# Performance work log

Measured on AMD Instinct MI355X. Metric: run time of the kernel, lower is better.

## Reference

```python
import jax, jax.numpy as jnp
import numpy as np

EPS = 1e-6
NUM_HEADS = 32
HEAD_DIM = 128


def _rms_norm(x, w):
    # RMSNorm over last dim (head_dim)
    var = jnp.mean(x * x, axis=-1, keepdims=True)
    return x * jax.lax.rsqrt(var + EPS) * w


def _rotate_half(x):
    x1, x2 = jnp.split(x, 2, axis=-1)
    return jnp.concatenate([-x2, x1], axis=-1)


def _apply_rope(x, cos, sin):
    # x: [b, t, h, d]; cos/sin: [t, d] -> broadcast over batch and heads
    c = cos[None, :, None, :]
    s = sin[None, :, None, :]
    return x * c + _rotate_half(x) * s


def setup_inputs() -> dict:
    key = jax.random.key(0)
    ks = jax.random.split(key, 7)
    b, q_len, ctx_len, hidden = 4, 64, 4096, 4096
    total = ctx_len + q_len
    return {
        "hidden_states": jax.random.normal(ks[0], (b, q_len, hidden), jnp.float32),
        "target_hidden": jax.random.normal(ks[1], (b, ctx_len, hidden), jnp.float32),
        "cos": jax.random.uniform(ks[2], (total, HEAD_DIM), jnp.float32, -1.0, 1.0),
        "sin": jax.random.uniform(ks[3], (total, HEAD_DIM), jnp.float32, -1.0, 1.0),
        "Wqkv": jax.random.normal(ks[4], (hidden, 3 * hidden), jnp.float32) * 0.02,
        "Wo": jax.random.normal(ks[5], (hidden, hidden), jnp.float32) * 0.02,
        "q_norm_w": jnp.ones((HEAD_DIM,), jnp.float32),
    }


def reference(hidden_states, target_hidden, cos, sin, Wqkv, Wo, q_norm_w):
    b, q_len, hidden = hidden_states.shape
    ctx_len = target_hidden.shape[1]
    H, D = NUM_HEADS, HEAD_DIM

    # fused QKV projection; only the query slice is consumed (per source)
    qkv = jnp.einsum("bqh,hz->bqz", hidden_states, Wqkv)
    q = qkv[..., : H * D].reshape(b, q_len, H, D)

    # q_norm is applied twice in the source forward
    q = _rms_norm(_rms_norm(q, q_norm_w), q_norm_w)

    # KV built by concatenating raw target_hidden context with draft hidden states
    kv = jnp.concatenate([target_hidden, hidden_states], axis=1)  # [b, ctx+q, hidden]
    k = kv.reshape(b, ctx_len + q_len, H, D)
    v = k  # v = k view per source (rope applied only to k)

    # rotary: draft queries occupy positions ctx_len .. ctx_len+q_len-1
    q = _apply_rope(q, cos[ctx_len:], sin[ctx_len:])
    k = _apply_rope(k, cos, sin)

    # attention (full attention of draft queries over context + draft keys)
    scale = 1.0 / jnp.sqrt(jnp.asarray(D, q.dtype))
    scores = jnp.einsum("bqhd,bkhd->bhqk", q, k) * scale
    probs = jax.nn.softmax(scores, axis=-1)
    out = jnp.einsum("bhqk,bkhd->bqhd", probs, v)

    out = out.reshape(b, q_len, H * D)
    return jnp.einsum("bqh,ho->bqo", out, Wo)
```

## Files before the change

kernel.cpp:

```cpp
#include <hip/hip_runtime.h>

typedef __attribute__((ext_vector_type(8))) short bf16x8;
typedef __attribute__((ext_vector_type(4))) float f32x4;
typedef __attribute__((ext_vector_type(4))) short s16x4;

#define DEV __device__ __forceinline__

DEV short f2bf(float f) {
  union { float f; unsigned u; } v; v.f = f;
  unsigned r = v.u + 0x7fffu + ((v.u >> 16) & 1u);
  return (short)(r >> 16);
}

DEV int pk2(float a, float b) {
#if defined(__has_builtin) && __has_builtin(__builtin_amdgcn_cvt_pk_bf16_f32)
  auto v = __builtin_amdgcn_cvt_pk_bf16_f32(a, b);
  int r; __builtin_memcpy(&r, &v, 4); return r;
#else
  return (int)(unsigned short)f2bf(a) | ((int)(unsigned short)f2bf(b) << 16);
#endif
}

DEV void stage16(const short* g, short* lbase, int lane) {
#if defined(__has_builtin) && __has_builtin(__builtin_amdgcn_global_load_lds)
  (void)lane;
  __builtin_amdgcn_global_load_lds((const __attribute__((address_space(1))) void*)g,
                                   (__attribute__((address_space(3))) void*)lbase, 16, 0, 0);
#else
  *(bf16x8*)(lbase + lane * 8) = *(const bf16x8*)g;
#endif
}

DEV void stage16f(const float* g, float* lbase, int lane) {
#if defined(__has_builtin) && __has_builtin(__builtin_amdgcn_global_load_lds)
  (void)lane;
  __builtin_amdgcn_global_load_lds((const __attribute__((address_space(1))) void*)g,
                                   (__attribute__((address_space(3))) void*)lbase, 16, 0, 0);
#else
  *(float4*)(lbase + lane * 4) = *(const float4*)g;
#endif
}

__global__ __launch_bounds__(256) void prep_w(
    const float* __restrict__ wqkv, const float* __restrict__ wo,
    short* __restrict__ out) {
  __shared__ short tile[64][66];
  int z = blockIdx.z;
  const float* in = z ? wo : wqkv;
  long ld = z ? 4096 : 12288;
  short* o = out + (long)z * 16777216L;
  long k0 = blockIdx.x * 64L, n0 = blockIdx.y * 64L;
  int t = threadIdx.x;
  {
    int kl = t >> 4, nl4 = (t & 15) * 4;
#pragma unroll
    for (int i = 0; i < 4; i++) {
      int k = kl + i * 16;
      float4 v = *(const float4*)(in + (k0 + k) * ld + n0 + nl4);
      int* dst = (int*)&tile[k][nl4];
      dst[0] = pk2(v.x, v.y);
      dst[1] = pk2(v.z, v.w);
    }
  }
  __syncthreads();
  {
    int nl = t >> 4, kl4 = (t & 15) * 4;
#pragma unroll
    for (int i = 0; i < 4; i++) {
      int n = nl + i * 16;
      s16x4 w;
      w.x = tile[kl4 + 0][n]; w.y = tile[kl4 + 1][n];
      w.z = tile[kl4 + 2][n]; w.w = tile[kl4 + 3][n];
      *(s16x4*)(o + (n0 + n) * 4096L + k0 + kl4) = w;
    }
  }
}

__global__ __launch_bounds__(256) void cast_f32_bf16(
    const float* __restrict__ in, short* __restrict__ out, int n8,
    float* __restrict__ zbuf) {
  int i = blockIdx.x * 256 + threadIdx.x;
  if (i >= n8) return;
  float4 a = *(const float4*)(in + (long)i * 8);
  float4 b = *(const float4*)(in + (long)i * 8 + 4);
  union { bf16x8 v; int w[4]; } r;
  r.w[0] = pk2(a.x, a.y); r.w[1] = pk2(a.z, a.w);
  r.w[2] = pk2(b.x, b.y); r.w[3] = pk2(b.z, b.w);
  *(bf16x8*)(out + (long)i * 8) = r.v;
  float4 z4 = make_float4(0.f, 0.f, 0.f, 0.f);
  *(float4*)(zbuf + (long)i * 8) = z4;
  *(float4*)(zbuf + (long)i * 8 + 4) = z4;
}

__global__ __launch_bounds__(512) void gemm_dma(
    const short* __restrict__ A, const short* __restrict__ Bt,
    float* __restrict__ Cp, int N, int K, int Kc) {
  __shared__ short As[32 * 512];
  __shared__ short Bs[8 * 512];
  int t = threadIdx.x;
  int lane = t & 63, wave = t >> 6;
  int quad = lane >> 4, m16 = lane & 15;
  long n0 = blockIdx.x * 64L;
  int z = blockIdx.y;
  f32x4 acc[2][4] = {};
  int kbeg = z * Kc, kend = kbeg + Kc;

  for (int k0 = kbeg; k0 < kend; k0 += 64) {
    __syncthreads();
#pragma unroll
    for (int i = 0; i < 2; i++)
#pragma unroll
      for (int s = 0; s < 2; s++) {
        int row = (2 * wave + i) * 16 + m16;
        const short* g = A + (long)row * K + k0 + (s * 4 + quad) * 8;
        stage16(g, &As[(4 * wave + 2 * i + s) * 512], lane);
      }
    {
      int nt = wave >> 1, s = wave & 1;
      long row = n0 + nt * 16 + m16;
      const short* g = Bt + row * (long)K + k0 + (s * 4 + quad) * 8;
      stage16(g, &Bs[wave * 512], lane);
    }
    __syncthreads();
#pragma unroll
    for (int s = 0; s < 2; s++) {
      bf16x8 a0 = *(bf16x8*)&As[(4 * wave + s) * 512 + lane * 8];
      bf16x8 a1 = *(bf16x8*)&As[(4 * wave + 2 + s) * 512 + lane * 8];
#pragma unroll
      for (int nt = 0; nt < 4; nt++) {
        bf16x8 b = *(bf16x8*)&Bs[(nt * 2 + s) * 512 + lane * 8];
        acc[0][nt] = __builtin_amdgcn_mfma_f32_16x16x32_bf16(a0, b, acc[0][nt], 0, 0, 0);
        acc[1][nt] = __builtin_amdgcn_mfma_f32_16x16x32_bf16(a1, b, acc[1][nt], 0, 0, 0);
      }
    }
  }
  float* C = Cp + (long)z * 256 * N;
#pragma unroll
  for (int i = 0; i < 2; i++)
#pragma unroll
    for (int nt = 0; nt < 4; nt++)
#pragma unroll
      for (int rg = 0; rg < 4; rg++) {
        long m = (2 * wave + i) * 16 + quad * 4 + rg;
        C[m * (long)N + n0 + nt * 16 + m16] = acc[i][nt][rg];
      }
}

__global__ __launch_bounds__(512) void gemm_dma_atomic(
    const short* __restrict__ A, const short* __restrict__ Bt,
    float* __restrict__ C, int N, int K, int Kc) {
  __shared__ short As[32 * 512];
  __shared__ short Bs[8 * 512];
  int t = threadIdx.x;
  int lane = t & 63, wave = t >> 6;
  int quad = lane >> 4, m16 = lane & 15;
  long n0 = blockIdx.x * 64L;
  int z = blockIdx.y;
  f32x4 acc[2][4] = {};
  int kbeg = z * Kc, kend = kbeg + Kc;

  for (int k0 = kbeg; k0 < kend; k0 += 64) {
    __syncthreads();
#pragma unroll
    for (int i = 0; i < 2; i++)
#pragma unroll
      for (int s = 0; s < 2; s++) {
        int row = (2 * wave + i) * 16 + m16;
        const short* g = A + (long)row * K + k0 + (s * 4 + quad) * 8;
        stage16(g, &As[(4 * wave + 2 * i + s) * 512], lane);
      }
    {
      int nt = wave >> 1, s = wave & 1;
      long row = n0 + nt * 16 + m16;
      const short* g = Bt + row * (long)K + k0 + (s * 4 + quad) * 8;
      stage16(g, &Bs[wave * 512], lane);
    }
    __syncthreads();
#pragma unroll
    for (int s = 0; s < 2; s++) {
      bf16x8 a0 = *(bf16x8*)&As[(4 * wave + s) * 512 + lane * 8];
      bf16x8 a1 = *(bf16x8*)&As[(4 * wave + 2 + s) * 512 + lane * 8];
#pragma unroll
      for (int nt = 0; nt < 4; nt++) {
        bf16x8 b = *(bf16x8*)&Bs[(nt * 2 + s) * 512 + lane * 8];
        acc[0][nt] = __builtin_amdgcn_mfma_f32_16x16x32_bf16(a0, b, acc[0][nt], 0, 0, 0);
        acc[1][nt] = __builtin_amdgcn_mfma_f32_16x16x32_bf16(a1, b, acc[1][nt], 0, 0, 0);
      }
    }
  }
#pragma unroll
  for (int i = 0; i < 2; i++)
#pragma unroll
    for (int nt = 0; nt < 4; nt++)
#pragma unroll
      for (int rg = 0; rg < 4; rg++) {
        long m = (2 * wave + i) * 16 + quad * 4 + rg;
        unsafeAtomicAdd(&C[m * (long)N + n0 + nt * 16 + m16], acc[i][nt][rg]);
      }
}

__global__ __launch_bounds__(256) void q_norm_rope(
    const float* __restrict__ qtmp, const float* __restrict__ qw,
    const float* __restrict__ cosp, const float* __restrict__ sinp,
    short* __restrict__ qr) {
  int wid = blockIdx.x * 4 + (threadIdx.x >> 6);
  int lane = threadIdx.x & 63;
  int rrow = wid >> 5, h = wid & 31;
  long base = (long)rrow * 4096 + h * 128;
  const long STR = 256L * 4096;
  float x1 = 0.f, x2 = 0.f;
#pragma unroll
  for (int z = 0; z < 8; z++) {
    x1 += qtmp[z * STR + base + lane];
    x2 += qtmp[z * STR + base + 64 + lane];
  }
  float w1 = qw[lane], w2 = qw[64 + lane];
  float ss = x1 * x1 + x2 * x2;
#pragma unroll
  for (int m = 1; m < 64; m <<= 1) ss += __shfl_xor(ss, m, 64);
  float rs = rsqrtf(ss * (1.0f / 128.0f) + 1e-6f);
  float y1 = x1 * rs * w1, y2 = x2 * rs * w2;
  float ss2 = y1 * y1 + y2 * y2;
#pragma unroll
  for (int m = 1; m < 64; m <<= 1) ss2 += __shfl_xor(ss2, m, 64);
  float rs2 = rsqrtf(ss2 * (1.0f / 128.0f) + 1e-6f);
  float z1 = y1 * rs2 * w1, z2 = y2 * rs2 * w2;
  long cpos = (long)(4096 + (rrow & 63)) * 128;
  float c1 = cosp[cpos + lane], c2 = cosp[cpos + 64 + lane];
  float s1 = sinp[cpos + lane], s2 = sinp[cpos + 64 + lane];
  const float scale = 0.08838834764831845f;
  float o1 = (z1 * c1 - z2 * s1) * scale;
  float o2 = (z2 * c2 + z1 * s2) * scale;
  qr[base + lane] = f2bf(o1);
  qr[base + 64 + lane] = f2bf(o2);
}

#define ATT_SPLIT 7
#define ATT_TILES 10

__global__ __launch_bounds__(256) void attn_kernel(
    const short* __restrict__ qr, const float* __restrict__ th,
    const float* __restrict__ hs, const float* __restrict__ cosp,
    const float* __restrict__ sinp, float* __restrict__ part,
    float* __restrict__ mstat, float* __restrict__ lstat) {
  __shared__ short Ks[64 * 136];
  __shared__ short Vt[128 * 80];
  __shared__ short Ps[64 * 72];
  __shared__ float Xraw[64 * 128];
  int bh = blockIdx.x, split = blockIdx.y;
  int b = bh >> 5, h = bh & 31;
  int t = threadIdx.x;
  int wave = t >> 6, lane = t & 63, quad = lane >> 4, m16 = lane & 15;

  int tile0 = split * ATT_TILES;
  int ntiles = (65 - tile0 < ATT_TILES) ? (65 - tile0) : ATT_TILES;

  bf16x8 aq[4];
  {
    const short* qrow = qr + (long)(b * 64 + wave * 16 + m16) * 4096 + h * 128;
#pragma unroll
    for (int s = 0; s < 4; s++) aq[s] = *(const bf16x8*)(qrow + s * 32 + quad * 8);
  }
  float mi[4] = {-INFINITY, -INFINITY, -INFINITY, -INFINITY};
  float li[4] = {0.f, 0.f, 0.f, 0.f};
  f32x4 oacc[8] = {};

  int srow = t >> 2;
  int sc = t & 3;
  int colw = srow ^ (sc * 16);

  {
    int tl = tile0;
#pragma unroll
    for (int j = 0; j < 8; j++) {
      int r = (wave * 8 + j) * 2 + (lane >> 5);
      int lgn = tl * 64 + r;
      int cs = lane & 31;
      int fo = (cs ^ (r & 7)) << 2;
      const float* src = (lgn < 4096)
          ? th + ((long)b * 4096 + lgn) * 4096 + h * 128 + fo
          : hs + ((long)b * 64 + (lgn - 4096)) * 4096 + h * 128 + fo;
      stage16f(src, &Xraw[(wave * 8 + j) * 256], lane);
    }
  }

  for (int tt = 0; tt < ntiles; tt++) {
    int lg = (tile0 + tt) * 64 + srow;
    __syncthreads();
    {
      const float* crow = cosp + (long)lg * 128;
      const float* srw = sinp + (long)lg * 128;
      const float* xrow = Xraw + srow * 128;
      int sx = srow & 7;
#pragma unroll
      for (int i = 0; i < 2; i++) {
        int c = sc + 4 * i;
        int d1 = c * 8, d2 = d1 + 64;
        int c0 = c * 2;
        alignas(16) float xa[8], xb[8], cA[8], sA[8], cB[8], sB[8];
        *(float4*)&xa[0] = *(const float4*)(xrow + ((c0 ^ sx) << 2));
        *(float4*)&xa[4] = *(const float4*)(xrow + (((c0 + 1) ^ sx) << 2));
        *(float4*)&xb[0] = *(const float4*)(xrow + (((c0 + 16) ^ sx) << 2));
        *(float4*)&xb[4] = *(const float4*)(xrow + (((c0 + 17) ^ sx) << 2));
        *(float4*)&cA[0] = *(const float4*)(crow + d1);
        *(float4*)&cA[4] = *(const float4*)(crow + d1 + 4);
        *(float4*)&cB[0] = *(const float4*)(crow + d2);
        *(float4*)&cB[4] = *(const float4*)(crow + d2 + 4);
        *(float4*)&sA[0] = *(const float4*)(srw + d1);
        *(float4*)&sA[4] = *(const float4*)(srw + d1 + 4);
        *(float4*)&sB[0] = *(const float4*)(srw + d2);
        *(float4*)&sB[4] = *(const float4*)(srw + d2 + 4);
        union { bf16x8 v; int w[4]; } K1, K2;
#pragma unroll
        for (int jj = 0; jj < 4; jj++) {
          int j0 = 2 * jj, j1 = 2 * jj + 1;
          K1.w[jj] = pk2(xa[j0] * cA[j0] - xb[j0] * sA[j0],
                         xa[j1] * cA[j1] - xb[j1] * sA[j1]);
          K2.w[jj] = pk2(xb[j0] * cB[j0] + xa[j0] * sB[j0],
                         xb[j1] * cB[j1] + xa[j1] * sB[j1]);
        }
        *(bf16x8*)&Ks[srow * 136 + d1] = K1.v;
        *(bf16x8*)&Ks[srow * 136 + d2] = K2.v;
#pragma unroll
        for (int jj = 0; jj < 4; jj++) {
          int p1 = pk2(xa[2 * jj], xa[2 * jj + 1]);
          int p2 = pk2(xb[2 * jj], xb[2 * jj + 1]);
          Vt[(d1 + 2 * jj) * 80 + colw] = (short)(p1 & 0xffff);
          Vt[(d1 + 2 * jj + 1) * 80 + colw] = (short)((unsigned)p1 >> 16);
          Vt[(d2 + 2 * jj) * 80 + colw] = (short)(p2 & 0xffff);
          Vt[(d2 + 2 * jj + 1) * 80 + colw] = (short)((unsigned)p2 >> 16);
        }
      }
    }
    __syncthreads();

    if (tt + 1 < ntiles) {
      int tl = tile0 + tt + 1;
#pragma unroll
      for (int j = 0; j < 8; j++) {
        int r = (wave * 8 + j) * 2 + (lane >> 5);
        int lgn = tl * 64 + r;
        int cs = lane & 31;
        int fo = (cs ^ (r & 7)) << 2;
        const float* src = (lgn < 4096)
            ? th + ((long)b * 4096 + lgn) * 4096 + h * 128 + fo
            : hs + ((long)b * 64 + (lgn - 4096)) * 4096 + h * 128 + fo;
        stage16f(src, &Xraw[(wave * 8 + j) * 256], lane);
      }
    }

    f32x4 sacc[4] = {};
#pragma unroll
    for (int s = 0; s < 4; s++)
#pragma unroll
      for (int nt = 0; nt < 4; nt++) {
        bf16x8 bk = *(const bf16x8*)&Ks[(nt * 16 + m16) * 136 + s * 32 + quad * 8];
        sacc[nt] = __builtin_amdgcn_mfma_f32_16x16x32_bf16(aq[s], bk, sacc[nt], 0, 0, 0);
      }

    float mnew[4], alpha[4];
#pragma unroll
    for (int rg = 0; rg < 4; rg++) {
      float mx = fmaxf(fmaxf(sacc[0][rg], sacc[1][rg]), fmaxf(sacc[2][rg], sacc[3][rg]));
#pragma unroll
      for (int msk = 1; msk < 16; msk <<= 1) mx = fmaxf(mx, __shfl_xor(mx, msk, 16));
      mnew[rg] = fmaxf(mi[rg], mx);
      alpha[rg] = __expf(mi[rg] - mnew[rg]);
      mi[rg] = mnew[rg];
    }
#pragma unroll
    for (int rg = 0; rg < 4; rg++) {
      float rs = 0.f;
#pragma unroll
      for (int nt = 0; nt < 4; nt++) {
        float p = __expf(sacc[nt][rg] - mnew[rg]);
        rs += p;
        Ps[(wave * 16 + quad * 4 + rg) * 72 + nt * 16 + m16] = f2bf(p);
      }
#pragma unroll
      for (int msk = 1; msk < 16; msk <<= 1) rs += __shfl_xor(rs, msk, 16);
      li[rg] = li[rg] * alpha[rg] + rs;
    }
#pragma unroll
    for (int nt = 0; nt < 8; nt++) {
      f32x4 o = oacc[nt];
      o[0] *= alpha[0]; o[1] *= alpha[1]; o[2] *= alpha[2]; o[3] *= alpha[3];
      oacc[nt] = o;
    }

    bf16x8 ap[2];
#pragma unroll
    for (int s = 0; s < 2; s++)
      ap[s] = *(const bf16x8*)&Ps[(wave * 16 + m16) * 72 + s * 32 + quad * 8];
#pragma unroll
    for (int s = 0; s < 2; s++)
#pragma unroll
      for (int nt = 0; nt < 8; nt++) {
        int d16 = nt * 16 + m16;
        int scd = (d16 >> 3) & 3;
        int cb = (s * 32 + quad * 8) ^ (scd * 16);
        bf16x8 bv = *(const bf16x8*)&Vt[d16 * 80 + cb];
        oacc[nt] = __builtin_amdgcn_mfma_f32_16x16x32_bf16(ap[s], bv, oacc[nt], 0, 0, 0);
      }
  }

  long pbase = (long)(bh * ATT_SPLIT + split) * 64;
#pragma unroll
  for (int nt = 0; nt < 8; nt++)
#pragma unroll
    for (int rg = 0; rg < 4; rg++)
      part[(pbase + wave * 16 + quad * 4 + rg) * 128 + nt * 16 + m16] = oacc[nt][rg];
  if (m16 == 0)
#pragma unroll
    for (int rg = 0; rg < 4; rg++) {
      mstat[pbase + wave * 16 + quad * 4 + rg] = mi[rg];
      lstat[pbase + wave * 16 + quad * 4 + rg] = li[rg];
    }
}

__global__ __launch_bounds__(128) void attn_merge(
    const float* __restrict__ part, const float* __restrict__ mstat,
    const float* __restrict__ lstat, short* __restrict__ attn) {
  int idx = blockIdx.x;
  int bh = idx >> 6, q = idx & 63;
  int d = threadIdx.x;
  float mstar = -INFINITY;
#pragma unroll
  for (int s = 0; s < ATT_SPLIT; s++)
    mstar = fmaxf(mstar, mstat[((long)bh * ATT_SPLIT + s) * 64 + q]);
  float denom = 0.f, o = 0.f;
#pragma unroll
  for (int s = 0; s < ATT_SPLIT; s++) {
    long sq = ((long)bh * ATT_SPLIT + s) * 64 + q;
    float w = __expf(mstat[sq] - mstar);
    denom += w * lstat[sq];
    o += w * part[sq * 128 + d];
  }
  int b = bh >> 5, h = bh & 31;
  attn[(long)(b * 64 + q) * 4096 + h * 128 + d] = f2bf(o / denom);
}

extern "C" void kernel_launch(void* const* d_in, const int* in_sizes, int n_in,
                              void* d_out, int out_size, void* d_ws, size_t ws_size,
                              hipStream_t stream) {
  const float* hs = (const float*)d_in[0];
  const float* th = (const float*)d_in[1];
  const float* cosp = (const float*)d_in[2];
  const float* sinp = (const float*)d_in[3];
  const float* wqkv = (const float*)d_in[4];
  const float* wo = (const float*)d_in[5];
  const float* qw = (const float*)d_in[6];
  float* out = (float*)d_out;

  char* ws = (char*)d_ws;
  short* WT   = (short*)ws;
  short* hsb  = (short*)(ws + (64L << 20));
  float* qtmp = (float*)(ws + (66L << 20));
  short* qrb  = (short*)(ws + (98L << 20));
  short* attnb= (short*)(ws + (100L << 20));
  float* part = (float*)(ws + (102L << 20));
  float* mstat= (float*)(ws + (131L << 20));
  float* lstat= (float*)(ws + (132L << 20));

  prep_w<<<dim3(64, 64, 2), 256, 0, stream>>>(wqkv, wo, WT);
  cast_f32_bf16<<<512, 256, 0, stream>>>(hs, hsb, 131072, out);
  gemm_dma<<<dim3(64, 8), 512, 0, stream>>>(hsb, WT, qtmp, 4096, 4096, 512);
  q_norm_rope<<<2048, 256, 0, stream>>>(qtmp, qw, cosp, sinp, qrb);
  attn_kernel<<<dim3(128, ATT_SPLIT), 256, 0, stream>>>(qrb, th, hs, cosp, sinp,
                                                        part, mstat, lstat);
  attn_merge<<<128 * 64, 128, 0, stream>>>(part, mstat, lstat, attnb);
  gemm_dma_atomic<<<dim3(64, 8), 512, 0, stream>>>(attnb, WT + 16777216L, out,
                                                   4096, 4096, 512);
}
```

Before: 631.5 us.

## Double-buffer split-K GEMM with atomics, remap blocks across XCDs, rebalance attention splits

The split-K GEMM now double-buffers its LDS tiles so the next K-chunk loads while MFMAs run on the current one. Both GEMMs accumulate through atomics into a zeroed buffer, which removes the 8-way partial buffer and the summation in q_norm_rope. Block IDs are remapped so consecutive blocks land on the same XCD, and attention goes from 7 splits of 10 tiles to 4 splits of 17. This trades extra LDS and atomic traffic for fewer partial writes and better overlap, and the remap assumes attn_merge handles the new split count.

```diff
diff --git a/kernel.cpp b/kernel.cpp
--- a/kernel.cpp
+++ b/kernel.cpp
@@ -78,7 +78,7 @@
 
 __global__ __launch_bounds__(256) void cast_f32_bf16(
     const float* __restrict__ in, short* __restrict__ out, int n8,
-    float* __restrict__ zbuf) {
+    float* __restrict__ z1, float* __restrict__ z2) {
   int i = blockIdx.x * 256 + threadIdx.x;
   if (i >= n8) return;
   float4 a = *(const float4*)(in + (long)i * 8);
@@ -88,106 +88,64 @@
   r.w[2] = pk2(b.x, b.y); r.w[3] = pk2(b.z, b.w);
   *(bf16x8*)(out + (long)i * 8) = r.v;
   float4 z4 = make_float4(0.f, 0.f, 0.f, 0.f);
-  *(float4*)(zbuf + (long)i * 8) = z4;
-  *(float4*)(zbuf + (long)i * 8 + 4) = z4;
-}
-
-__global__ __launch_bounds__(512) void gemm_dma(
+  *(float4*)(z1 + (long)i * 8) = z4;
+  *(float4*)(z1 + (long)i * 8 + 4) = z4;
+  *(float4*)(z2 + (long)i * 8) = z4;
+  *(float4*)(z2 + (long)i * 8 + 4) = z4;
+}
+
+__global__ __launch_bounds__(512) void gemm_dma_at(
     const short* __restrict__ A, const short* __restrict__ Bt,
-    float* __restrict__ Cp, int N, int K, int Kc) {
-  __shared__ short As[32 * 512];
-  __shared__ short Bs[8 * 512];
+    float* __restrict__ C, int N, int K, int Kc) {
+  __shared__ short As[2][32 * 512];
+  __shared__ short Bs[2][8 * 512];
   int t = threadIdx.x;
   int lane = t & 63, wave = t >> 6;
   int quad = lane >> 4, m16 = lane & 15;
-  long n0 = blockIdx.x * 64L;
-  int z = blockIdx.y;
+  int sid = (blockIdx.x & 7) * 64 + (blockIdx.x >> 3);
+  int z = sid >> 6;
+  long n0 = (sid & 63) * 64L;
   f32x4 acc[2][4] = {};
-  int kbeg = z * Kc, kend = kbeg + Kc;
-
-  for (int k0 = kbeg; k0 < kend; k0 += 64) {
+  int kbeg = z * Kc;
+  int niter = Kc / 64;
+
+#define GSTAGE(B, K0)                                                        \
+  {                                                                          \
+    _Pragma("unroll")                                                        \
+    for (int i = 0; i < 2; i++)                                              \
+      _Pragma("unroll")                                                      \
+      for (int s = 0; s < 2; s++) {                                          \
+        int row = (2 * wave + i) * 16 + m16;                                 \
+        const short* g = A + (long)row * K + (K0) + (s * 4 + quad) * 8;      \
+        stage16(g, &As[B][(4 * wave + 2 * i + s) * 512], lane);              \
+      }                                                                      \
+    {                                                                        \
+      int nt = wave >> 1, s = wave & 1;                                      \
+      long row = n0 + nt * 16 + m16;                                         \
+      const short* g = Bt + row * (long)K + (K0) + (s * 4 + quad) * 8;       \
+      stage16(g, &Bs[B][wave * 512], lane);                                  \
+    }                                                                        \
+  }
+
+  GSTAGE(0, kbeg);
+  int cur = 0;
+  for (int it = 0; it < niter; ++it) {
     __syncthreads();
-#pragma unroll
-    for (int i = 0; i < 2; i++)
-#pragma unroll
-      for (int s = 0; s < 2; s++) {
-        int row = (2 * wave + i) * 16 + m16;
-        const short* g = A + (long)row * K + k0 + (s * 4 + quad) * 8;
-        stage16(g, &As[(4 * wave + 2 * i + s) * 512], lane);
-      }
-    {
-      int nt = wave >> 1, s = wave & 1;
-      long row = n0 + nt * 16 + m16;
-      const short* g = Bt + row * (long)K + k0 + (s * 4 + quad) * 8;
-      stage16(g, &Bs[wave * 512], lane);
-    }
-    __syncthreads();
+    if (it + 1 < niter) GSTAGE(cur ^ 1, kbeg + (it + 1) * 64);
 #pragma unroll
     for (int s = 0; s < 2; s++) {
-      bf16x8 a0 = *(bf16x8*)&As[(4 * wave + s) * 512 + lane * 8];
-      bf16x8 a1 = *(bf16x8*)&As[(4 * wave + 2 + s) * 512 + lane * 8];
+      bf16x8 a0 = *(bf16x8*)&As[cur][(4 * wave + s) * 512 + lane * 8];
+      bf16x8 a1 = *(bf16x8*)&As[cur][(4 * wave + 2 + s) * 512 + lane * 8];
 #pragma unroll
       for (int nt = 0; nt < 4; nt++) {
-        bf16x8 b = *(bf16x8*)&Bs[(nt * 2 + s) * 512 + lane * 8];
+        bf16x8 b = *(bf16x8*)&Bs[cur][(nt * 2 + s) * 512 + lane * 8];
         acc[0][nt] = __builtin_amdgcn_mfma_f32_16x16x32_bf16(a0, b, acc[0][nt], 0, 0, 0);
         acc[1][nt] = __builtin_amdgcn_mfma_f32_16x16x32_bf16(a1, b, acc[1][nt], 0, 0, 0);
       }
     }
-  }
-  float* C = Cp + (long)z * 256 * N;
-#pragma unroll
-  for (int i = 0; i < 2; i++)
-#pragma unroll
-    for (int nt = 0; nt < 4; nt++)
-#pragma unroll
-      for (int rg = 0; rg < 4; rg++) {
-        long m = (2 * wave + i) * 16 + quad * 4 + rg;
-        C[m * (long)N + n0 + nt * 16 + m16] = acc[i][nt][rg];
-      }
-}
-
-__global__ __launch_bounds__(512) void gemm_dma_atomic(
-    const short* __restrict__ A, const short* __restrict__ Bt,
-    float* __restrict__ C, int N, int K, int Kc) {
-  __shared__ short As[32 * 512];
-  __shared__ short Bs[8 * 512];
-  int t = threadIdx.x;
-  int lane = t & 63, wave = t >> 6;
-  int quad = lane >> 4, m16 = lane & 15;
-  long n0 = blockIdx.x * 64L;
-  int z = blockIdx.y;
-  f32x4 acc[2][4] = {};
-  int kbeg = z * Kc, kend = kbeg + Kc;
-
-  for (int k0 = kbeg; k0 < kend; k0 += 64) {
-    __syncthreads();
-#pragma unroll
-    for (int i = 0; i < 2; i++)
-#pragma unroll
-      for (int s = 0; s < 2; s++) {
-        int row = (2 * wave + i) * 16 + m16;
-        const short* g = A + (long)row * K + k0 + (s * 4 + quad) * 8;
-        stage16(g, &As[(4 * wave + 2 * i + s) * 512], lane);
-      }
-    {
-      int nt = wave >> 1, s = wave & 1;
-      long row = n0 + nt * 16 + m16;
-      const short* g = Bt + row * (long)K + k0 + (s * 4 + quad) * 8;
-      stage16(g, &Bs[wave * 512], lane);
-    }
-    __syncthreads();
-#pragma unroll
-    for (int s = 0; s < 2; s++) {
-      bf16x8 a0 = *(bf16x8*)&As[(4 * wave + s) * 512 + lane * 8];
-      bf16x8 a1 = *(bf16x8*)&As[(4 * wave + 2 + s) * 512 + lane * 8];
-#pragma unroll
-      for (int nt = 0; nt < 4; nt++) {
-        bf16x8 b = *(bf16x8*)&Bs[(nt * 2 + s) * 512 + lane * 8];
-        acc[0][nt] = __builtin_amdgcn_mfma_f32_16x16x32_bf16(a0, b, acc[0][nt], 0, 0, 0);
-        acc[1][nt] = __builtin_amdgcn_mfma_f32_16x16x32_bf16(a1, b, acc[1][nt], 0, 0, 0);
-      }
-    }
-  }
+    cur ^= 1;
+  }
+#undef GSTAGE
 #pragma unroll
   for (int i = 0; i < 2; i++)
 #pragma unroll
@@ -207,13 +165,8 @@
   int lane = threadIdx.x & 63;
   int rrow = wid >> 5, h = wid & 31;
   long base = (long)rrow * 4096 + h * 128;
-  const long STR = 256L * 4096;
-  float x1 = 0.f, x2 = 0.f;
-#pragma unroll
-  for (int z = 0; z < 8; z++) {
-    x1 += qtmp[z * STR + base + lane];
-    x2 += qtmp[z * STR + base + 64 + lane];
-  }
+  float x1 = qtmp[base + lane];
+  float x2 = qtmp[base + 64 + lane];
   float w1 = qw[lane], w2 = qw[64 + lane];
   float ss = x1 * x1 + x2 * x2;
 #pragma unroll
@@ -235,8 +188,8 @@
   qr[base + 64 + lane] = f2bf(o2);
 }
 
-#define ATT_SPLIT 7
-#define ATT_TILES 10
+#define ATT_SPLIT 4
+#define ATT_TILES 17
 
 __global__ __launch_bounds__(256) void attn_kernel(
     const short* __restrict__ qr, const float* __restrict__ th,
@@ -247,7 +200,8 @@
   __shared__ short Vt[128 * 80];
   __shared__ short Ps[64 * 72];
   __shared__ float Xraw[64 * 128];
-  int bh = blockIdx.x, split = blockIdx.y;
+  int sid = (blockIdx.x & 7) * 64 + (blockIdx.x >> 3);
+  int bh = sid & 127, split = sid >> 7;
   int b = bh >> 5, h = bh & 31;
   int t = threadIdx.x;
   int wave = t >> 6, lane = t & 63, quad = lane >> 4, m16 = lane & 15;
@@ -456,19 +410,19 @@
   short* WT   = (short*)ws;
   short* hsb  = (short*)(ws + (64L << 20));
   float* qtmp = (float*)(ws + (66L << 20));
-  short* qrb  = (short*)(ws + (98L << 20));
-  short* attnb= (short*)(ws + (100L << 20));
-  float* part = (float*)(ws + (102L << 20));
-  float* mstat= (float*)(ws + (131L << 20));
-  float* lstat= (float*)(ws + (132L << 20));
+  short* qrb  = (short*)(ws + (70L << 20));
+  short* attnb= (short*)(ws + (72L << 20));
+  float* part = (float*)(ws + (74L << 20));
+  float* mstat= (float*)(ws + (90L << 20));
+  float* lstat= (float*)(ws + (91L << 20));
 
   prep_w<<<dim3(64, 64, 2), 256, 0, stream>>>(wqkv, wo, WT);
-  cast_f32_bf16<<<512, 256, 0, stream>>>(hs, hsb, 131072, out);
-  gemm_dma<<<dim3(64, 8), 512, 0, stream>>>(hsb, WT, qtmp, 4096, 4096, 512);
+  cast_f32_bf16<<<512, 256, 0, stream>>>(hs, hsb, 131072, qtmp, out);
+  gemm_dma_at<<<512, 512, 0, stream>>>(hsb, WT, qtmp, 4096, 4096, 512);
   q_norm_rope<<<2048, 256, 0, stream>>>(qtmp, qw, cosp, sinp, qrb);
-  attn_kernel<<<dim3(128, ATT_SPLIT), 256, 0, stream>>>(qrb, th, hs, cosp, sinp,
-                                                        part, mstat, lstat);
+  attn_kernel<<<512, 256, 0, stream>>>(qrb, th, hs, cosp, sinp,
+                                       part, mstat, lstat);
   attn_merge<<<128 * 64, 128, 0, stream>>>(part, mstat, lstat, attnb);
-  gemm_dma_atomic<<<dim3(64, 8), 512, 0, stream>>>(attnb, WT + 16777216L, out,
-                                                   4096, 4096, 512);
-}
+  gemm_dma_at<<<512, 512, 0, stream>>>(attnb, WT + 16777216L, out,
+                                       4096, 4096, 512);
+}
```

New measurement: 659.3 us. +4.4%, slower.
